# Optimization experiments

Measured on AMD Instinct MI355X. Metric: run time of the kernel, lower is better.

## Reference

```python
import jax, jax.numpy as jnp
import numpy as np

B = 65536; T = 7
N_NUM = 32; N_CAT = 16; CARD = 100; D_CAT = 16
D_STATE = 96; D_HID = 192; S_DIM = 64; DT = 1.0
D_IN = N_NUM + N_CAT * D_CAT + 8  # 296
D_Z = 3 * D_STATE + 64            # 352

def _ln(x, g, b, eps=1e-5):
    m = x.mean(-1, keepdims=True)
    v = ((x - m) ** 2).mean(-1, keepdims=True)
    return (x - m) * jax.lax.rsqrt(v + eps) * g + b

def _gelu(x):
    return jax.nn.gelu(x, approximate=False)  # matches torch F.gelu default (erf)

def _forward(x_num, x_static, cat_emb, day_emb, xproj_w, xproj_b, h0,
             bln_g, bln_b, fc1_w, fc1_b, fc2_w, fc2_b,
             spln_g, spln_b, sp1_w, sp1_b, sp2_w, sp2_b,
             base_w, base_b, hln_g, hln_b,
             hm1_w, hm1_b, hm2_w, hm2_b,
             hq1_w, hq1_b, hq2_w, hq2_b,
             hn1_w, hn1_b, hn2_w, hn2_b, x_cat):
    Bsz = x_num.shape[0]
    # categorical embeddings: per-feature table lookup -> (B,T,N_CAT,D_CAT)
    emb = jax.vmap(lambda tab, idx: tab[idx], in_axes=(0, 2), out_axes=2)(cat_emb, x_cat)
    emb = emb.reshape(Bsz, T, N_CAT * D_CAT)
    # day ids are arange(1,8), shared over batch
    day = jnp.broadcast_to(day_emb[1:8], (Bsz, T, 8))
    x = jnp.concatenate([x_num, emb, day], axis=-1)          # (B,T,D_IN)
    x = x @ xproj_w + xproj_b                                # (B,T,D_STATE)

    def step(h, xt):  # Euler-integrated LN+MLP residual cell (dropout = eval identity)
        z = jnp.concatenate([h, xt], axis=-1)                # (B,2*D_STATE)
        z = _ln(z, bln_g, bln_b)
        dh = _gelu(z @ fc1_w + fc1_b) @ fc2_w + fc2_b
        h = h + DT * dh
        return h, h

    h0b = jnp.broadcast_to(h0, (Bsz, D_STATE))
    _, hs = jax.lax.scan(step, h0b, jnp.swapaxes(x, 0, 1))   # (T,B,D_STATE)
    H = jnp.swapaxes(hs, 0, 1)                               # (B,T,D_STATE)
    h_last = H[:, -1]
    h_mean = H.mean(axis=1)
    h_max = H.max(axis=1)

    s = _ln(x_static, spln_g, spln_b)
    s64 = _gelu(s @ sp1_w + sp1_b) @ sp2_w + sp2_b           # (B,64)

    z = jnp.concatenate([h_last, h_mean, h_max, s64], axis=-1)  # (B,D_Z)
    z = _ln(z, hln_g, hln_b)
    base = x_static @ base_w + base_b                        # (B,)
    mean = base + _gelu(z @ hm1_w + hm1_b) @ hm2_w + hm2_b
    q20 = base + _gelu(z @ hq1_w + hq1_b) @ hq2_w + hq2_b
    neg_logit = _gelu(z @ hn1_w + hn1_b) @ hn2_w + hn2_b
    return mean, q20, neg_logit

def setup_inputs() -> dict:
    key = jax.random.key(0)
    ks = iter(jax.random.split(key, 64))
    def w(shape, scale=0.02):
        return (scale * jax.random.normal(next(ks), shape)).astype(jnp.float32)
    def zz(shape):
        return jnp.zeros(shape, jnp.float32)
    def oo(shape):
        return jnp.ones(shape, jnp.float32)
    inp = {
        "x_num": jax.random.normal(next(ks), (B, T, N_NUM), jnp.float32),
        "x_static": jax.random.normal(next(ks), (B, S_DIM), jnp.float32),
        "x_cat": jax.random.randint(next(ks), (B, T, N_CAT), 0, CARD),
        "cat_emb": w((N_CAT, CARD + 1, D_CAT), 1.0),
        "day_emb": w((8, 8), 1.0),
        "xproj_w": w((D_IN, D_STATE)), "xproj_b": zz((D_STATE,)),
        "h0": zz((D_STATE,)),
        "bln_g": oo((2 * D_STATE,)), "bln_b": zz((2 * D_STATE,)),
        "fc1_w": w((2 * D_STATE, D_HID)), "fc1_b": zz((D_HID,)),
        "fc2_w": w((D_HID, D_STATE)), "fc2_b": zz((D_STATE,)),
        "spln_g": oo((S_DIM,)), "spln_b": zz((S_DIM,)),
        "sp1_w": w((S_DIM, 128)), "sp1_b": zz((128,)),
        "sp2_w": w((128, 64)), "sp2_b": zz((64,)),
        "base_w": w((S_DIM,)), "base_b": zz(()),
        "hln_g": oo((D_Z,)), "hln_b": zz((D_Z,)),
        "hm1_w": w((D_Z, D_HID)), "hm1_b": zz((D_HID,)),
        "hm2_w": w((D_HID,)), "hm2_b": zz(()),
        "hq1_w": w((D_Z, D_HID)), "hq1_b": zz((D_HID,)),
        "hq2_w": w((D_HID,)), "hq2_b": zz(()),
        "hn1_w": w((D_Z, D_HID // 2)), "hn1_b": zz((D_HID // 2,)),
        "hn2_w": w((D_HID // 2,)), "hn2_b": zz(()),
    }
    return inp

def reference(x_num, x_static, x_cat, cat_emb, day_emb, xproj_w, xproj_b, h0,
              bln_g, bln_b, fc1_w, fc1_b, fc2_w, fc2_b,
              spln_g, spln_b, sp1_w, sp1_b, sp2_w, sp2_b,
              base_w, base_b, hln_g, hln_b,
              hm1_w, hm1_b, hm2_w, hm2_b,
              hq1_w, hq1_b, hq2_w, hq2_b,
              hn1_w, hn1_b, hn2_w, hn2_b):
    return _forward(x_num, x_static, cat_emb, day_emb, xproj_w, xproj_b, h0,
                    bln_g, bln_b, fc1_w, fc1_b, fc2_w, fc2_b,
                    spln_g, spln_b, sp1_w, sp1_b, sp2_w, sp2_b,
                    base_w, base_b, hln_g, hln_b,
                    hm1_w, hm1_b, hm2_w, hm2_b,
                    hq1_w, hq1_b, hq2_w, hq2_b,
                    hn1_w, hn1_b, hn2_w, hn2_b, x_cat)
```

## Files before the change

kernel.cpp:

```cpp
#include <hip/hip_runtime.h>
#include <math.h>

#define NB 65536

typedef __attribute__((ext_vector_type(8))) short bf16x8;
typedef __attribute__((ext_vector_type(4))) float f32x4;

#define O_BIAST  0
#define O_FC1C   4096
#define O_FC1BP  8192
#define O_FC1FR  12288
#define O_FC2FR  86016
#define O_HDFR   122880
#define O_HDC    460800
#define O_HDBP   462848
#define O_W2C    464896
#define O_SPC    466944
#define O_SPB    467968
#define O_SP1FR  468992
#define O_SP2FR  485376
#define O_XP2FR  501760
#define O_EMB16  557056
#define O_FEAT   608768
#define O_S64    38357504
#define O_STAT   46746112
#define O_BASE   47270400
#define O_XROW   47532544
#define O_XSTAT  135612928

__device__ __forceinline__ unsigned short f2b(float x) {
  unsigned int u = __float_as_uint(x);
  u += 0x7fffu + ((u >> 16) & 1u);
  return (unsigned short)(u >> 16);
}
__device__ __forceinline__ float b2f(unsigned short u) {
  return __uint_as_float(((unsigned)u) << 16);
}
__device__ __forceinline__ float geluf(float x) {
  float z = x * x;
  float e = __builtin_amdgcn_exp2f(-x * (2.3022137f + 0.10294456f * z));
  return x * __builtin_amdgcn_rcpf(1.0f + e);
}

__device__ __forceinline__ void head_fold_part(
    int part, int tid,
    const float* __restrict__ hln_g, const float* __restrict__ hln_b,
    const float* __restrict__ hm1_w, const float* __restrict__ hm1_b,
    const float* __restrict__ hq1_w, const float* __restrict__ hq1_b,
    const float* __restrict__ hn1_w, const float* __restrict__ hn1_b,
    const float* __restrict__ hm2_w, const float* __restrict__ hq2_w,
    const float* __restrict__ hn2_w, char* __restrict__ wsb)
{
  if (tid >= 480) return;
  const int gcol = part*120 + (tid >> 2);
  const int ksl = tid & 3;
  float C = 0.f, Bp = 0.f;
  for (int j = 0; j < 88; ++j) {
    int k = ksl*88 + j;
    float w;
    if (gcol < 192) w = hm1_w[k*192 + gcol];
    else if (gcol < 384) w = hq1_w[k*192 + (gcol-192)];
    else w = hn1_w[k*96 + (gcol-384)];
    C = fmaf(hln_g[k], w, C);
    Bp = fmaf(hln_b[k], w, Bp);
  }
  C += __shfl_xor(C, 1, 64); C += __shfl_xor(C, 2, 64);
  Bp += __shfl_xor(Bp, 1, 64); Bp += __shfl_xor(Bp, 2, 64);
  if (ksl == 0) {
    float b0, w2;
    if (gcol < 192) { b0 = hm1_b[gcol]; w2 = hm2_w[gcol]; }
    else if (gcol < 384) { b0 = hq1_b[gcol-192]; w2 = hq2_w[gcol-192]; }
    else { b0 = hn1_b[gcol-384]; w2 = hn2_w[gcol-384]; }
    ((float*)(wsb + O_HDC))[gcol] = C;
    ((float*)(wsb + O_HDBP))[gcol] = Bp + b0;
    ((float*)(wsb + O_W2C))[gcol] = w2;
  }
}

__global__ void k0_pre(
    const float* __restrict__ cat_emb, const float* __restrict__ day_emb,
    const float* __restrict__ xproj_w, const float* __restrict__ xproj_b,
    const float* __restrict__ bln_g, const float* __restrict__ bln_b,
    const float* __restrict__ fc1_w, const float* __restrict__ fc1_b,
    const float* __restrict__ fc2_w,
    const float* __restrict__ spln_g, const float* __restrict__ spln_b,
    const float* __restrict__ sp1_w, const float* __restrict__ sp1_b,
    const float* __restrict__ sp2_w,
    const float* __restrict__ hln_g, const float* __restrict__ hln_b,
    const float* __restrict__ hm1_w, const float* __restrict__ hm1_b,
    const float* __restrict__ hq1_w, const float* __restrict__ hq1_b,
    const float* __restrict__ hn1_w, const float* __restrict__ hn1_b,
    const float* __restrict__ hm2_w, const float* __restrict__ hq2_w,
    const float* __restrict__ hn2_w,
    char* __restrict__ wsb)
{
  const int b = blockIdx.x, tid = threadIdx.x;
  if (b < 7) {
    if (tid < 96) {
      int t = b;
      float acc = xproj_b[tid];
      #pragma unroll
      for (int d = 0; d < 8; ++d)
        acc = fmaf(day_emb[(1+t)*8 + d], xproj_w[(288+d)*96 + tid], acc);
      ((float*)(wsb + O_BIAST))[t*96 + tid] = acc;
    }
  } else if (b < 9) {
    if (tid < 384) {
      int col = (b-7)*96 + (tid >> 2);
      int ksl = tid & 3;
      float C = 0.f, Bp = 0.f;
      for (int j = 0; j < 48; ++j) {
        int k = ksl*48 + j;
        float w = fc1_w[k*192 + col];
        C = fmaf(bln_g[k], w, C);
        Bp = fmaf(bln_b[k], w, Bp);
      }
      C += __shfl_xor(C, 1, 64); C += __shfl_xor(C, 2, 64);
      Bp += __shfl_xor(Bp, 1, 64); Bp += __shfl_xor(Bp, 2, 64);
      if (ksl == 0) {
        ((float*)(wsb + O_FC1C))[col] = C;
        ((float*)(wsb + O_FC1BP))[col] = Bp + fc1_b[col];
      }
    }
  } else if (b < 81) {
    int seg = b - 9, nt = seg / 6, ks = seg - nt*6;
    int ln = tid >> 3, j = tid & 7;
    int k = ks*32 + (ln>>4)*8 + j, col = nt*16 + (ln&15);
    ((unsigned short*)(wsb + O_FC1FR))[(seg*64 + ln)*8 + j] = f2b(bln_g[k]*fc1_w[k*192 + col]);
  } else if (b < 117) {
    int seg = b - 81, nt = seg / 6, ks = seg - nt*6;
    int ln = tid >> 3, j = tid & 7;
    int k = ks*32 + (ln>>4)*8 + j, col = nt*16 + (ln&15);
    ((unsigned short*)(wsb + O_FC2FR))[(seg*64 + ln)*8 + j] = f2b(fc2_w[k*96 + col]);
  } else if (b < 447) {
    int seg = b - 117, nt = seg / 11, ks = seg - nt*11;
    int ln = tid >> 3, j = tid & 7;
    int k = ks*32 + (ln>>4)*8 + j, gcol = nt*16 + (ln&15);
    float w;
    if (gcol < 192) w = hm1_w[k*192 + gcol];
    else if (gcol < 384) w = hq1_w[k*192 + (gcol-192)];
    else w = hn1_w[k*96 + (gcol-384)];
    ((unsigned short*)(wsb + O_HDFR))[(seg*64 + ln)*8 + j] = f2b(hln_g[k]*w);
  } else if (b < 448) {
    head_fold_part(0, tid, hln_g, hln_b, hm1_w, hm1_b, hq1_w, hq1_b,
                   hn1_w, hn1_b, hm2_w, hq2_w, hn2_w, wsb);
  } else if (b < 449) {
    if (tid < 128) {
      int col = tid;
      float C = 0.f, Bp = sp1_b[col];
      for (int k = 0; k < 64; ++k) {
        float w = sp1_w[k*128 + col];
        C += b2f(f2b(spln_g[k]*w));
        Bp = fmaf(spln_b[k], w, Bp);
      }
      ((float*)(wsb + O_SPC))[col] = C;
      ((float*)(wsb + O_SPB))[col] = Bp;
    }
  } else if (b < 465) {
    int seg = b - 449;
    int ln = tid >> 3, j = tid & 7;
    int nt = seg >> 1, ks = seg & 1;
    int k = ks*32 + (ln>>4)*8 + j, col = nt*16 + (ln&15);
    ((unsigned short*)(wsb + O_SP1FR))[(seg*64 + ln)*8 + j] = f2b(spln_g[k]*sp1_w[k*128 + col]);
  } else if (b < 481) {
    int seg = b - 465;
    int ln = tid >> 3, j = tid & 7;
    int ks = seg & 3;
    int k = ks*32 + (ln>>4)*8 + j, col = (seg >> 2)*16 + (ln&15);
    ((unsigned short*)(wsb + O_SP2FR))[(seg*64 + ln)*8 + j] = f2b(sp2_w[k*64 + col]);
  } else if (b < 535) {
    int seg = b - 481, ks = seg / 6, nt = seg - ks*6;
    int ln = tid >> 3, j = tid & 7;
    int k = ks*32 + (ln>>4)*8 + j, col = nt*16 + (ln&15);
    ((unsigned short*)(wsb + O_XP2FR))[(seg*64 + ln)*8 + j] = f2b(xproj_w[k*96 + col]);
  } else if (b < 586) {
    int i = (b - 535)*512 + tid;
    if (i < 25856)
      ((unsigned short*)(wsb + O_EMB16))[i] = f2b(cat_emb[i]);
  } else {
    head_fold_part(b - 585, tid, hln_g, hln_b, hm1_w, hm1_b, hq1_w, hq1_b,
                   hn1_w, hn1_b, hm2_w, hq2_w, hn2_w, wsb);
  }
}

__global__ __launch_bounds__(256) void k1ab(
    const float* __restrict__ x_num, const int* __restrict__ x_cat,
    const float* __restrict__ x_static, const float* __restrict__ sp2_b,
    const float* __restrict__ base_w, const float* __restrict__ base_b,
    char* __restrict__ wsb, unsigned short* __restrict__ xrow,
    float* __restrict__ xstat)
{
  __shared__ char smem[28288];
  const int tid = threadIdx.x;
  const int wv = tid >> 6, l = tid & 63, lr = l & 15, lq = l >> 4;
  const f32x4 zero4 = {0.f, 0.f, 0.f, 0.f};

  if (blockIdx.x >= 3584) {
    unsigned short* hid = (unsigned short*)smem;
    const int srow = (blockIdx.x - 3584)*64 + wv*16;

    float x0f[8], x1f[8];
    {
      const float* xr = x_static + (size_t)(srow + lr)*64;
      *(float4*)&x0f[0] = *(const float4*)(xr + lq*8);
      *(float4*)&x0f[4] = *(const float4*)(xr + lq*8 + 4);
      *(float4*)&x1f[0] = *(const float4*)(xr + 32 + lq*8);
      *(float4*)&x1f[4] = *(const float4*)(xr + 32 + lq*8 + 4);
    }
    float sm = 0.f, sq = 0.f, bp = 0.f;
    #pragma unroll
    for (int j = 0; j < 8; ++j) {
      sm += x0f[j] + x1f[j];
      sq = fmaf(x0f[j], x0f[j], fmaf(x1f[j], x1f[j], sq));
      bp = fmaf(x0f[j], base_w[lq*8 + j], fmaf(x1f[j], base_w[32 + lq*8 + j], bp));
    }
    sm += __shfl_xor(sm, 16, 64); sm += __shfl_xor(sm, 32, 64);
    sq += __shfl_xor(sq, 16, 64); sq += __shfl_xor(sq, 32, 64);
    bp += __shfl_xor(bp, 16, 64); bp += __shfl_xor(bp, 32, 64);
    if (lq == 0) ((float*)(wsb + O_BASE))[srow + lr] = bp + base_b[0];
    const float ms = sm*(1.f/64.f);
    const float rs = rsqrtf(sq*(1.f/64.f) - ms*ms + 1e-5f);
    float mr[4], rr[4];
    #pragma unroll
    for (int i = 0; i < 4; ++i) {
      mr[i] = __shfl(ms, lq*4 + i, 16);
      rr[i] = __shfl(rs, lq*4 + i, 16);
    }
    union { bf16x8 v; unsigned short u[8]; } ua0, ua1;
    #pragma unroll
    for (int j = 0; j < 8; ++j) { ua0.u[j] = f2b(x0f[j]); ua1.u[j] = f2b(x1f[j]); }

    const bf16x8* f1 = (const bf16x8*)(wsb + O_SP1FR);
    const bf16x8* f2 = (const bf16x8*)(wsb + O_SP2FR);
    unsigned short* hw = hid + wv*2176;

    f32x4 acc[8];
    #pragma unroll
    for (int nt = 0; nt < 8; ++nt) acc[nt] = zero4;
    #pragma unroll
    for (int nt = 0; nt < 8; ++nt) {
      acc[nt] = __builtin_amdgcn_mfma_f32_16x16x32_bf16(ua0.v, f1[(nt*2 + 0)*64 + l], acc[nt], 0, 0, 0);
      acc[nt] = __builtin_amdgcn_mfma_f32_16x16x32_bf16(ua1.v, f1[(nt*2 + 1)*64 + l], acc[nt], 0, 0, 0);
    }
    {
      const float* spC = (const float*)(wsb + O_SPC);
      const float* spB = (const float*)(wsb + O_SPB);
      #pragma unroll
      for (int nt = 0; nt < 8; ++nt) {
        float Cv = spC[nt*16 + lr], Bv = spB[nt*16 + lr];
        #pragma unroll
        for (int i = 0; i < 4; ++i) {
          float hv = rr[i]*(acc[nt][i] - mr[i]*Cv) + Bv;
          hw[(lq*4 + i)*136 + nt*16 + lr] = f2b(geluf(hv));
        }
      }
    }
    f32x4 a2[4];
    #pragma unroll
    for (int nt = 0; nt < 4; ++nt) a2[nt] = zero4;
    #pragma unroll
    for (int ks = 0; ks < 4; ++ks) {
      bf16x8 a = *(const bf16x8*)(hw + lr*136 + ks*32 + lq*8);
      #pragma unroll
      for (int nt = 0; nt < 4; ++nt)
        a2[nt] = __builtin_amdgcn_mfma_f32_16x16x32_bf16(a, f2[(nt*4 + ks)*64 + l], a2[nt], 0, 0, 0);
    }
    float ss[4] = {0.f,0.f,0.f,0.f}, qq[4] = {0.f,0.f,0.f,0.f};
    {
      unsigned short* s64p = (unsigned short*)(wsb + O_S64);
      #pragma unroll
      for (int nt = 0; nt < 4; ++nt) {
        float bv = sp2_b[nt*16 + lr];
        #pragma unroll
        for (int i = 0; i < 4; ++i) {
          unsigned short rb = f2b(a2[nt][i] + bv);
          s64p[(size_t)(srow + lq*4 + i)*64 + nt*16 + lr] = rb;
          float f = b2f(rb);
          ss[i] += f; qq[i] = fmaf(f, f, qq[i]);
        }
      }
    }
    #pragma unroll
    for (int i = 0; i < 4; ++i) {
      ss[i] += __shfl_xor(ss[i], 1, 64); ss[i] += __shfl_xor(ss[i], 2, 64);
      ss[i] += __shfl_xor(ss[i], 4, 64); ss[i] += __shfl_xor(ss[i], 8, 64);
      qq[i] += __shfl_xor(qq[i], 1, 64); qq[i] += __shfl_xor(qq[i], 2, 64);
      qq[i] += __shfl_xor(qq[i], 4, 64); qq[i] += __shfl_xor(qq[i], 8, 64);
    }
    if (lr == 0) {
      float* stat = (float*)(wsb + O_STAT);
      #pragma unroll
      for (int i = 0; i < 4; ++i) {
        size_t r = (size_t)srow + lq*4 + i;
        float2 o; o.x = ss[i]; o.y = qq[i];
        *(float2*)(stat + r*2) = o;
      }
    }
    return;
  }

  float (*ctile)[16][100] = (float(*)[16][100])smem;
  float (*bsh)[96] = (float(*)[96])(smem + 25600);
  const unsigned ctA = blockIdx.x*128u + wv*32u + lr;
  const unsigned ctB = ctA + 16u;
  const int lqh = lq >> 1, lql = lq & 1;

  if (tid < 168)
    ((float4*)bsh)[tid] = ((const float4*)(wsb + O_BIAST))[tid];
  __syncthreads();

  int eA[8], eB[8];
  {
    const int4* ip = (const int4*)(x_cat + (size_t)ctA*16);
    int4 v0 = ip[0], v1 = ip[1], v2 = ip[2], v3 = ip[3];
    eA[0] = lqh ? v0.y : v0.x;  eA[1] = lqh ? v0.w : v0.z;
    eA[2] = lqh ? v1.y : v1.x;  eA[3] = lqh ? v1.w : v1.z;
    eA[4] = lqh ? v2.y : v2.x;  eA[5] = lqh ? v2.w : v2.z;
    eA[6] = lqh ? v3.y : v3.x;  eA[7] = lqh ? v3.w : v3.z;
  }
  {
    const int4* ip = (const int4*)(x_cat + (size_t)ctB*16);
    int4 v0 = ip[0], v1 = ip[1], v2 = ip[2], v3 = ip[3];
    eB[0] = lqh ? v0.y : v0.x;  eB[1] = lqh ? v0.w : v0.z;
    eB[2] = lqh ? v1.y : v1.x;  eB[3] = lqh ? v1.w : v1.z;
    eB[4] = lqh ? v2.y : v2.x;  eB[5] = lqh ? v2.w : v2.z;
    eB[6] = lqh ? v3.y : v3.x;  eB[7] = lqh ? v3.w : v3.z;
  }
  const unsigned short* emb = (const unsigned short*)(wsb + O_EMB16);
  const bf16x8* xp2 = (const bf16x8*)(wsb + O_XP2FR);
  f32x4 accA[6], accB[6];
  #pragma unroll
  for (int nt = 0; nt < 6; ++nt) { accA[nt] = zero4; accB[nt] = zero4; }

  {
    union { bf16x8 v; unsigned short u[8]; } auA, auB;
    {
      const float* xa = x_num + (size_t)ctA*32 + lq*8;
      const float* xb = x_num + (size_t)ctB*32 + lq*8;
      float fa[8], fb[8];
      *(float4*)&fa[0] = *(const float4*)xa;
      *(float4*)&fa[4] = *(const float4*)(xa + 4);
      *(float4*)&fb[0] = *(const float4*)xb;
      *(float4*)&fb[4] = *(const float4*)(xb + 4);
      #pragma unroll
      for (int j = 0; j < 8; ++j) { auA.u[j] = f2b(fa[j]); auB.u[j] = f2b(fb[j]); }
    }
    #pragma unroll
    for (int nt = 0; nt < 6; ++nt) {
      bf16x8 w = xp2[nt*64 + l];
      accA[nt] = __builtin_amdgcn_mfma_f32_16x16x32_bf16(auA.v, w, accA[nt], 0, 0, 0);
      accB[nt] = __builtin_amdgcn_mfma_f32_16x16x32_bf16(auB.v, w, accB[nt], 0, 0, 0);
    }
  }
  #pragma unroll
  for (int c2 = 0; c2 < 8; ++c2) {
    bf16x8 aA = *(const bf16x8*)(emb + ((c2*2+lqh)*101 + eA[c2])*16 + lql*8);
    bf16x8 aB = *(const bf16x8*)(emb + ((c2*2+lqh)*101 + eB[c2])*16 + lql*8);
    #pragma unroll
    for (int nt = 0; nt < 6; ++nt) {
      bf16x8 w = xp2[((c2+1)*6+nt)*64 + l];
      accA[nt] = __builtin_amdgcn_mfma_f32_16x16x32_bf16(aA, w, accA[nt], 0, 0, 0);
      accB[nt] = __builtin_amdgcn_mfma_f32_16x16x32_bf16(aB, w, accB[nt], 0, 0, 0);
    }
  }

  #pragma unroll
  for (int nt = 0; nt < 6; ++nt) {
    #pragma unroll
    for (int i = 0; i < 4; ++i)
      ctile[wv][lq*4 + i][nt*16 + lr] = accA[nt][i];
  }
  asm volatile("s_waitcnt lgkmcnt(0)" ::: "memory");
  __builtin_amdgcn_sched_barrier(0);
  {
    const unsigned t = ctA % 7u;
    float cv[24], bv[24];
    #pragma unroll
    for (int q = 0; q < 6; ++q) {
      *(float4*)&cv[q*4] = *(const float4*)&ctile[wv][lr][lq*24 + q*4];
      *(float4*)&bv[q*4] = *(const float4*)&bsh[t][lq*24 + q*4];
    }
    unsigned ow[12];
    float sm = 0.f, sq = 0.f;
    #pragma unroll
    for (int u = 0; u < 12; ++u) {
      unsigned short u0 = f2b(cv[2*u]   + bv[2*u]);
      unsigned short u1 = f2b(cv[2*u+1] + bv[2*u+1]);
      ow[u] = (unsigned)u0 | ((unsigned)u1 << 16);
      float f0 = b2f(u0), f1 = b2f(u1);
      sm += f0 + f1; sq = fmaf(f0, f0, fmaf(f1, f1, sq));
    }
    {
      uint4* xo = (uint4*)(xrow + (size_t)ctA*96 + lq*24);
      xo[0] = make_uint4(ow[0], ow[1], ow[2], ow[3]);
      xo[1] = make_uint4(ow[4], ow[5], ow[6], ow[7]);
      xo[2] = make_uint4(ow[8], ow[9], ow[10], ow[11]);
    }
    sm += __shfl_xor(sm, 16, 64); sm += __shfl_xor(sm, 32, 64);
    sq += __shfl_xor(sq, 16, 64); sq += __shfl_xor(sq, 32, 64);
    if (lq == 0) {
      float2 o; o.x = sm; o.y = sq;
      *(float2*)(xstat + (size_t)ctA*2) = o;
    }
  }
  asm volatile("s_waitcnt lgkmcnt(0)" ::: "memory");
  __builtin_amdgcn_sched_barrier(0);
  #pragma unroll
  for (int nt = 0; nt < 6; ++nt) {
    #pragma unroll
    for (int i = 0; i < 4; ++i)
      ctile[wv][lq*4 + i][nt*16 + lr] = accB[nt][i];
  }
  asm volatile("s_waitcnt lgkmcnt(0)" ::: "memory");
  __builtin_amdgcn_sched_barrier(0);
  {
    const unsigned t = ctB % 7u;
    float cv[24], bv[24];
    #pragma unroll
    for (int q = 0; q < 6; ++q) {
      *(float4*)&cv[q*4] = *(const float4*)&ctile[wv][lr][lq*24 + q*4];
      *(float4*)&bv[q*4] = *(const float4*)&bsh[t][lq*24 + q*4];
    }
    unsigned ow[12];
    float sm = 0.f, sq = 0.f;
    #pragma unroll
    for (int u = 0; u < 12; ++u) {
      unsigned short u0 = f2b(cv[2*u]   + bv[2*u]);
      unsigned short u1 = f2b(cv[2*u+1] + bv[2*u+1]);
      ow[u] = (unsigned)u0 | ((unsigned)u1 << 16);
      float f0 = b2f(u0), f1 = b2f(u1);
      sm += f0 + f1; sq = fmaf(f0, f0, fmaf(f1, f1, sq));
    }
    {
      uint4* xo = (uint4*)(xrow + (size_t)ctB*96 + lq*24);
      xo[0] = make_uint4(ow[0], ow[1], ow[2], ow[3]);
      xo[1] = make_uint4(ow[4], ow[5], ow[6], ow[7]);
      xo[2] = make_uint4(ow[8], ow[9], ow[10], ow[11]);
    }
    sm += __shfl_xor(sm, 16, 64); sm += __shfl_xor(sm, 32, 64);
    sq += __shfl_xor(sq, 16, 64); sq += __shfl_xor(sq, 32, 64);
    if (lq == 0) {
      float2 o; o.x = sm; o.y = sq;
      *(float2*)(xstat + (size_t)ctB*2) = o;
    }
  }
}

__global__ __launch_bounds__(512, 2) void k1_scan(
    const float* __restrict__ h0, const float* __restrict__ fc2_b,
    const char* __restrict__ wsb, const unsigned short* __restrict__ xrow,
    const float* __restrict__ xstat, unsigned short* __restrict__ feat,
    float* __restrict__ statg)
{
  extern __shared__ char smem[];
  unsigned short* zg = (unsigned short*)smem;
  unsigned short* f1f = (unsigned short*)(smem + 51200);
  unsigned short* f2f = (unsigned short*)(smem + 124928);

  const int tid = threadIdx.x;
  const int wv = tid >> 6;
  const int l = tid & 63;
  const int lr = l & 15;
  const int lq = l >> 4;
  const int rowt = wv*16 + lr;

  {
    const uint4* s1 = (const uint4*)(wsb + O_FC1FR);
    uint4* d1 = (uint4*)f1f;
    for (int o = tid; o < 4608; o += 512) d1[o] = s1[o];
    const uint4* s2 = (const uint4*)(wsb + O_FC2FR);
    uint4* d2 = (uint4*)f2f;
    for (int o = tid; o < 2304; o += 512) d2[o] = s2[o];
  }
  const bf16x8* f1v = (const bf16x8*)f1f;
  const bf16x8* f2v = (const bf16x8*)f2f;

  float C1[12], B1[12];
  {
    const float* fc1C = (const float*)(wsb + O_FC1C);
    const float* fc1BP = (const float*)(wsb + O_FC1BP);
    #pragma unroll
    for (int nt = 0; nt < 12; ++nt) { C1[nt] = fc1C[nt*16+lr]; B1[nt] = fc1BP[nt*16+lr]; }
  }
  float fb2[6];
  #pragma unroll
  for (int nt = 0; nt < 6; ++nt) fb2[nt] = fc2_b[nt*16+lr];

  float h[24], hs[24], hm[24];
  #pragma unroll
  for (int nt = 0; nt < 6; ++nt) {
    float v = h0[nt*16+lr];
    #pragma unroll
    for (int i = 0; i < 4; ++i) { h[nt*4+i] = v; hs[nt*4+i] = 0.f; hm[nt*4+i] = -3.4e38f; }
  }
  __syncthreads();

  const f32x4 zero4 = {0.f, 0.f, 0.f, 0.f};
  const size_t srow_q = (size_t)blockIdx.x*128 + wv*16;

  for (int t = 0; t < 7; ++t) {
    float hsm[4] = {0.f,0.f,0.f,0.f}, hsq[4] = {0.f,0.f,0.f,0.f};
    #pragma unroll
    for (int nt = 0; nt < 6; ++nt) {
      #pragma unroll
      for (int i = 0; i < 4; ++i) {
        unsigned short hb = f2b(h[nt*4+i]);
        zg[(wv*16 + lq*4 + i)*200 + nt*16 + lr] = hb;
        float hf = b2f(hb);
        hsm[i] += hf; hsq[i] = fmaf(hf, hf, hsq[i]);
      }
    }
    #pragma unroll
    for (int i = 0; i < 4; ++i) {
      hsm[i] += __shfl_xor(hsm[i], 1, 64); hsm[i] += __shfl_xor(hsm[i], 2, 64);
      hsm[i] += __shfl_xor(hsm[i], 4, 64); hsm[i] += __shfl_xor(hsm[i], 8, 64);
      hsq[i] += __shfl_xor(hsq[i], 1, 64); hsq[i] += __shfl_xor(hsq[i], 2, 64);
      hsq[i] += __shfl_xor(hsq[i], 4, 64); hsq[i] += __shfl_xor(hsq[i], 8, 64);
    }
    float mr[4], rr[4];
    #pragma unroll
    for (int i = 0; i < 4; ++i) {
      const float2 xs = *(const float2*)(xstat + ((srow_q + lq*4 + i)*7 + t)*2);
      float m = (hsm[i] + xs.x) * (1.f/192.f);
      float var = (hsq[i] + xs.y) * (1.f/192.f) - m*m;
      mr[i] = m; rr[i] = rsqrtf(var + 1e-5f);
    }
    bf16x8 ax[3];
    {
      const unsigned short* xp = xrow + ((srow_q + lr)*7 + t)*96;
      #pragma unroll
      for (int k3 = 0; k3 < 3; ++k3)
        ax[k3] = *(const bf16x8*)(xp + k3*32 + lq*8);
    }
    f32x4 acc[12];
    #pragma unroll
    for (int nt = 0; nt < 12; ++nt) acc[nt] = zero4;
    #pragma unroll
    for (int ks = 0; ks < 3; ++ks) {
      bf16x8 a = *(const bf16x8*)(zg + rowt*200 + ks*32 + lq*8);
      #pragma unroll
      for (int nt = 0; nt < 12; ++nt)
        acc[nt] = __builtin_amdgcn_mfma_f32_16x16x32_bf16(a, f1v[(nt*6+ks)*64 + l], acc[nt], 0, 0, 0);
    }
    #pragma unroll
    for (int k3 = 0; k3 < 3; ++k3) {
      #pragma unroll
      for (int nt = 0; nt < 12; ++nt)
        acc[nt] = __builtin_amdgcn_mfma_f32_16x16x32_bf16(ax[k3], f1v[(nt*6+k3+3)*64 + l], acc[nt], 0, 0, 0);
    }
    #pragma unroll
    for (int nt = 0; nt < 12; ++nt) {
      #pragma unroll
      for (int i = 0; i < 4; ++i) {
        float hid = rr[i]*(acc[nt][i] - mr[i]*C1[nt]) + B1[nt];
        zg[(wv*16 + lq*4 + i)*200 + nt*16 + lr] = f2b(geluf(hid));
      }
    }
    f32x4 a2[6];
    #pragma unroll
    for (int nt = 0; nt < 6; ++nt) a2[nt] = zero4;
    #pragma unroll
    for (int ks = 0; ks < 6; ++ks) {
      bf16x8 a = *(const bf16x8*)(zg + rowt*200 + ks*32 + lq*8);
      #pragma unroll
      for (int nt = 0; nt < 6; ++nt)
        a2[nt] = __builtin_amdgcn_mfma_f32_16x16x32_bf16(a, f2v[(nt*6+ks)*64 + l], a2[nt], 0, 0, 0);
    }
    #pragma unroll
    for (int nt = 0; nt < 6; ++nt) {
      #pragma unroll
      for (int i = 0; i < 4; ++i) {
        int u = nt*4 + i;
        h[u] += a2[nt][i] + fb2[nt];
        hs[u] += h[u];
        hm[u] = fmaxf(hm[u], h[u]);
      }
    }
  }
  float st[4] = {0.f,0.f,0.f,0.f}, qt[4] = {0.f,0.f,0.f,0.f};
  #pragma unroll
  for (int nt = 0; nt < 6; ++nt) {
    #pragma unroll
    for (int i = 0; i < 4; ++i) {
      size_t r = (srow_q + lq*4 + i)*288;
      int c = nt*16 + lr;
      unsigned short b0 = f2b(h[nt*4+i]);
      unsigned short b1 = f2b(hs[nt*4+i]*(1.f/7.f));
      unsigned short b2v = f2b(hm[nt*4+i]);
      feat[r + c] = b0;
      feat[r + 96 + c] = b1;
      feat[r + 192 + c] = b2v;
      float f0 = b2f(b0), f1 = b2f(b1), f2v = b2f(b2v);
      st[i] += f0 + f1 + f2v;
      qt[i] = fmaf(f0, f0, fmaf(f1, f1, fmaf(f2v, f2v, qt[i])));
    }
  }
  #pragma unroll
  for (int i = 0; i < 4; ++i) {
    st[i] += __shfl_xor(st[i], 1, 64); st[i] += __shfl_xor(st[i], 2, 64);
    st[i] += __shfl_xor(st[i], 4, 64); st[i] += __shfl_xor(st[i], 8, 64);
    qt[i] += __shfl_xor(qt[i], 1, 64); qt[i] += __shfl_xor(qt[i], 2, 64);
    qt[i] += __shfl_xor(qt[i], 4, 64); qt[i] += __shfl_xor(qt[i], 8, 64);
  }
  if (lr == 0) {
    #pragma unroll
    for (int i = 0; i < 4; ++i) {
      size_t r = srow_q + lq*4 + i;
      float2 fs = *(float2*)(statg + r*2);
      float stot = fs.x + st[i], qtot = fs.y + qt[i];
      float m = stot*(1.f/352.f);
      float var = qtot*(1.f/352.f) - m*m;
      float2 o; o.x = m; o.y = rsqrtf(var + 1e-5f);
      *(float2*)(statg + r*2) = o;
    }
  }
}

__global__ __launch_bounds__(512, 2) void k2b_heads(
    const float* __restrict__ hm2_b, const float* __restrict__ hq2_b,
    const float* __restrict__ hn2_b, const char* __restrict__ wsb,
    const unsigned short* __restrict__ feat, float* __restrict__ out)
{
  extern __shared__ char smem[];
  const int g = blockIdx.y;
  const int tid = threadIdx.x;
  const int wv = tid >> 6, l = tid & 63, lr = l & 15, lq = l >> 4;
  const int ntn = (g == 2) ? 6 : 12;
  {
    const uint4* src = (const uint4*)(wsb + O_HDFR + (size_t)g*135168);
    uint4* dst = (uint4*)smem;
    const int n = ntn*11*64;
    for (int o = tid; o < n; o += 512) dst[o] = src[o];
  }
  __syncthreads();
  const bf16x8* wfr = (const bf16x8*)smem;
  const float* hdC = (const float*)(wsb + O_HDC);
  const float* hdB = (const float*)(wsb + O_HDBP);
  const float* w2c = (const float*)(wsb + O_W2C);
  const float* stat = (const float*)(wsb + O_STAT);
  const float* baseb = (const float*)(wsb + O_BASE);
  const unsigned short* s64p = (const unsigned short*)(wsb + O_S64);
  const float hb = (g == 0) ? hm2_b[0] : (g == 1) ? hq2_b[0] : hn2_b[0];
  const f32x4 zero4 = {0.f, 0.f, 0.f, 0.f};

  for (int c = blockIdx.x; c < 256; c += gridDim.x) {
    const int base = c*256 + wv*32;
    bf16x8 afr0[11], afr1[11];
    {
      const unsigned short* fr0 = feat + (size_t)(base + lr)*288;
      const unsigned short* fr1 = feat + (size_t)(base + 16 + lr)*288;
      #pragma unroll
      for (int ks = 0; ks < 9; ++ks) {
        afr0[ks] = *(const bf16x8*)(fr0 + ks*32 + lq*8);
        afr1[ks] = *(const bf16x8*)(fr1 + ks*32 + lq*8);
      }
      const unsigned short* sr0 = s64p + (size_t)(base + lr)*64;
      const unsigned short* sr1 = s64p + (size_t)(base + 16 + lr)*64;
      afr0[9]  = *(const bf16x8*)(sr0 + lq*8);
      afr0[10] = *(const bf16x8*)(sr0 + 32 + lq*8);
      afr1[9]  = *(const bf16x8*)(sr1 + lq*8);
      afr1[10] = *(const bf16x8*)(sr1 + 32 + lq*8);
    }
    float mr0[4], rr0[4], mr1[4], rr1[4];
    #pragma unroll
    for (int i = 0; i < 4; ++i) {
      float2 s0 = *(const float2*)(stat + (size_t)(base + lq*4 + i)*2);
      float2 s1 = *(const float2*)(stat + (size_t)(base + 16 + lq*4 + i)*2);
      mr0[i] = s0.x; rr0[i] = s0.y; mr1[i] = s1.x; rr1[i] = s1.y;
    }
    float pr0[4] = {0.f,0.f,0.f,0.f}, pr1[4] = {0.f,0.f,0.f,0.f};
    for (int nt = 0; nt < ntn; ++nt) {
      const int col = (g*12 + nt)*16 + lr;
      const float Cv = hdC[col], Bv = hdB[col], w2v = w2c[col];
      f32x4 a0 = zero4, a1v = zero4;
      #pragma unroll
      for (int ks = 0; ks < 11; ++ks) {
        bf16x8 b = wfr[(nt*11 + ks)*64 + l];
        a0  = __builtin_amdgcn_mfma_f32_16x16x32_bf16(afr0[ks], b, a0, 0, 0, 0);
        a1v = __builtin_amdgcn_mfma_f32_16x16x32_bf16(afr1[ks], b, a1v, 0, 0, 0);
      }
      #pragma unroll
      for (int i = 0; i < 4; ++i) {
        pr0[i] += geluf(rr0[i]*(a0[i]  - mr0[i]*Cv) + Bv) * w2v;
        pr1[i] += geluf(rr1[i]*(a1v[i] - mr1[i]*Cv) + Bv) * w2v;
      }
    }
    #pragma unroll
    for (int i = 0; i < 4; ++i) {
      float v0 = pr0[i], v1 = pr1[i];
      v0 += __shfl_xor(v0, 1, 64); v0 += __shfl_xor(v0, 2, 64);
      v0 += __shfl_xor(v0, 4, 64); v0 += __shfl_xor(v0, 8, 64);
      v1 += __shfl_xor(v1, 1, 64); v1 += __shfl_xor(v1, 2, 64);
      v1 += __shfl_xor(v1, 4, 64); v1 += __shfl_xor(v1, 8, 64);
      if (lr == 0) {
        int r0 = base + lq*4 + i;
        int r1 = base + 16 + lq*4 + i;
        float b0 = (g < 2) ? baseb[r0] : 0.f;
        float b1 = (g < 2) ? baseb[r1] : 0.f;
        out[(size_t)g*NB + r0] = b0 + hb + v0;
        out[(size_t)g*NB + r1] = b1 + hb + v1;
      }
    }
  }
}

extern "C" void kernel_launch(void* const* d_in, const int* in_sizes, int n_in,
                              void* d_out, int out_size, void* d_ws, size_t ws_size,
                              hipStream_t stream) {
  (void)in_sizes; (void)n_in; (void)out_size; (void)ws_size;
  const float* x_num    = (const float*)d_in[0];
  const float* x_static = (const float*)d_in[1];
  const int*   x_cat    = (const int*)  d_in[2];
  const float* cat_emb  = (const float*)d_in[3];
  const float* day_emb  = (const float*)d_in[4];
  const float* xproj_w  = (const float*)d_in[5];
  const float* xproj_b  = (const float*)d_in[6];
  const float* h0       = (const float*)d_in[7];
  const float* bln_g    = (const float*)d_in[8];
  const float* bln_b    = (const float*)d_in[9];
  const float* fc1_w    = (const float*)d_in[10];
  const float* fc1_b    = (const float*)d_in[11];
  const float* fc2_w    = (const float*)d_in[12];
  const float* fc2_b    = (const float*)d_in[13];
  const float* spln_g   = (const float*)d_in[14];
  const float* spln_b   = (const float*)d_in[15];
  const float* sp1_w    = (const float*)d_in[16];
  const float* sp1_b    = (const float*)d_in[17];
  const float* sp2_w    = (const float*)d_in[18];
  const float* sp2_b    = (const float*)d_in[19];
  const float* base_w   = (const float*)d_in[20];
  const float* base_b   = (const float*)d_in[21];
  const float* hln_g    = (const float*)d_in[22];
  const float* hln_b    = (const float*)d_in[23];
  const float* hm1_w    = (const float*)d_in[24];
  const float* hm1_b    = (const float*)d_in[25];
  const float* hm2_w    = (const float*)d_in[26];
  const float* hm2_b    = (const float*)d_in[27];
  const float* hq1_w    = (const float*)d_in[28];
  const float* hq1_b    = (const float*)d_in[29];
  const float* hq2_w    = (const float*)d_in[30];
  const float* hq2_b    = (const float*)d_in[31];
  const float* hn1_w    = (const float*)d_in[32];
  const float* hn1_b    = (const float*)d_in[33];
  const float* hn2_w    = (const float*)d_in[34];
  const float* hn2_b    = (const float*)d_in[35];

  char* wsb = (char*)d_ws;
  unsigned short* feat = (unsigned short*)(wsb + O_FEAT);
  unsigned short* xrow = (unsigned short*)(wsb + O_XROW);
  float* xstat = (float*)(wsb + O_XSTAT);
  float* statg = (float*)(wsb + O_STAT);
  float* out = (float*)d_out;

  k0_pre<<<589, 512, 0, stream>>>(cat_emb, day_emb, xproj_w, xproj_b,
      bln_g, bln_b, fc1_w, fc1_b, fc2_w, spln_g, spln_b, sp1_w, sp1_b, sp2_w,
      hln_g, hln_b, hm1_w, hm1_b, hq1_w, hq1_b, hn1_w, hn1_b,
      hm2_w, hq2_w, hn2_w, wsb);
  k1ab<<<4608, 256, 0, stream>>>(x_num, x_cat, x_static, sp2_b, base_w, base_b,
      wsb, xrow, xstat);
  k1_scan<<<512, 512, 161792, stream>>>(h0, fc2_b, wsb, xrow, xstat, feat, statg);
  k2b_heads<<<dim3(64, 3), 512, 135168, stream>>>(hm2_b, hq2_b, hn2_b,
      wsb, feat, out);
}
```

Baseline: 278.6 us.

## Fuse prediction heads into scan kernel via shared-memory feature tile

Moves the three head MLPs into the end of the scan kernel. The pooled hidden features and the static embedding are staged per row in shared memory instead of being written to global memory and re-read by a separate heads kernel. Head weight fragments are now read directly from global or L2 rather than staged in LDS, and each wave computes all 30 output column tiles for its 16 rows. This removes a kernel launch and the round trip of the feature buffer through memory. In exchange there is no LDS reuse of the head weights and less row blocking per weight load.

```diff
diff --git a/kernel.cpp b/kernel.cpp
--- a/kernel.cpp
+++ b/kernel.cpp
@@ -448,9 +448,11 @@
 
 __global__ __launch_bounds__(512, 2) void k1_scan(
     const float* __restrict__ h0, const float* __restrict__ fc2_b,
+    const float* __restrict__ hm2_b, const float* __restrict__ hq2_b,
+    const float* __restrict__ hn2_b,
     const char* __restrict__ wsb, const unsigned short* __restrict__ xrow,
-    const float* __restrict__ xstat, unsigned short* __restrict__ feat,
-    float* __restrict__ statg)
+    const float* __restrict__ xstat, float* __restrict__ statg,
+    float* __restrict__ out)
 {
   extern __shared__ char smem[];
   unsigned short* zg = (unsigned short*)smem;
@@ -577,23 +579,33 @@
       }
     }
   }
+
+  __syncthreads();
+  unsigned short* zt = (unsigned short*)smem;
   float st[4] = {0.f,0.f,0.f,0.f}, qt[4] = {0.f,0.f,0.f,0.f};
   #pragma unroll
   for (int nt = 0; nt < 6; ++nt) {
     #pragma unroll
     for (int i = 0; i < 4; ++i) {
-      size_t r = (srow_q + lq*4 + i)*288;
+      int row = wv*16 + lq*4 + i;
       int c = nt*16 + lr;
       unsigned short b0 = f2b(h[nt*4+i]);
       unsigned short b1 = f2b(hs[nt*4+i]*(1.f/7.f));
       unsigned short b2v = f2b(hm[nt*4+i]);
-      feat[r + c] = b0;
-      feat[r + 96 + c] = b1;
-      feat[r + 192 + c] = b2v;
-      float f0 = b2f(b0), f1 = b2f(b1), f2v = b2f(b2v);
-      st[i] += f0 + f1 + f2v;
-      qt[i] = fmaf(f0, f0, fmaf(f1, f1, fmaf(f2v, f2v, qt[i])));
-    }
+      zt[row*360 + c] = b0;
+      zt[row*360 + 96 + c] = b1;
+      zt[row*360 + 192 + c] = b2v;
+      float f0 = b2f(b0), f1 = b2f(b1), f2x = b2f(b2v);
+      st[i] += f0 + f1 + f2x;
+      qt[i] = fmaf(f0, f0, fmaf(f1, f1, fmaf(f2x, f2x, qt[i])));
+    }
+  }
+  {
+    const unsigned short* s64p = (const unsigned short*)(wsb + O_S64);
+    const uint4* sp = (const uint4*)(s64p + (srow_q + lr)*64 + lq*16);
+    uint4 v0 = sp[0], v1 = sp[1];
+    *(uint4*)(zt + (wv*16 + lr)*360 + 288 + lq*16) = v0;
+    *(uint4*)(zt + (wv*16 + lr)*360 + 288 + lq*16 + 8) = v1;
   }
   #pragma unroll
   for (int i = 0; i < 4; ++i) {
@@ -602,104 +614,56 @@
     qt[i] += __shfl_xor(qt[i], 1, 64); qt[i] += __shfl_xor(qt[i], 2, 64);
     qt[i] += __shfl_xor(qt[i], 4, 64); qt[i] += __shfl_xor(qt[i], 8, 64);
   }
-  if (lr == 0) {
-    #pragma unroll
-    for (int i = 0; i < 4; ++i) {
-      size_t r = srow_q + lq*4 + i;
-      float2 fs = *(float2*)(statg + r*2);
-      float stot = fs.x + st[i], qtot = fs.y + qt[i];
-      float m = stot*(1.f/352.f);
-      float var = qtot*(1.f/352.f) - m*m;
-      float2 o; o.x = m; o.y = rsqrtf(var + 1e-5f);
-      *(float2*)(statg + r*2) = o;
-    }
-  }
-}
-
-__global__ __launch_bounds__(512, 2) void k2b_heads(
-    const float* __restrict__ hm2_b, const float* __restrict__ hq2_b,
-    const float* __restrict__ hn2_b, const char* __restrict__ wsb,
-    const unsigned short* __restrict__ feat, float* __restrict__ out)
-{
-  extern __shared__ char smem[];
-  const int g = blockIdx.y;
-  const int tid = threadIdx.x;
-  const int wv = tid >> 6, l = tid & 63, lr = l & 15, lq = l >> 4;
-  const int ntn = (g == 2) ? 6 : 12;
-  {
-    const uint4* src = (const uint4*)(wsb + O_HDFR + (size_t)g*135168);
-    uint4* dst = (uint4*)smem;
-    const int n = ntn*11*64;
-    for (int o = tid; o < n; o += 512) dst[o] = src[o];
-  }
-  __syncthreads();
-  const bf16x8* wfr = (const bf16x8*)smem;
+  float mr[4], rr[4];
+  #pragma unroll
+  for (int i = 0; i < 4; ++i) {
+    const float2 fs = *(const float2*)(statg + (srow_q + lq*4 + i)*2);
+    float stot = fs.x + st[i], qtot = fs.y + qt[i];
+    float m = stot*(1.f/352.f);
+    float var = qtot*(1.f/352.f) - m*m;
+    mr[i] = m; rr[i] = rsqrtf(var + 1e-5f);
+  }
+  const bf16x8* hv = (const bf16x8*)(wsb + O_HDFR);
   const float* hdC = (const float*)(wsb + O_HDC);
   const float* hdB = (const float*)(wsb + O_HDBP);
   const float* w2c = (const float*)(wsb + O_W2C);
-  const float* stat = (const float*)(wsb + O_STAT);
-  const float* baseb = (const float*)(wsb + O_BASE);
-  const unsigned short* s64p = (const unsigned short*)(wsb + O_S64);
-  const float hb = (g == 0) ? hm2_b[0] : (g == 1) ? hq2_b[0] : hn2_b[0];
-  const f32x4 zero4 = {0.f, 0.f, 0.f, 0.f};
-
-  for (int c = blockIdx.x; c < 256; c += gridDim.x) {
-    const int base = c*256 + wv*32;
-    bf16x8 afr0[11], afr1[11];
-    {
-      const unsigned short* fr0 = feat + (size_t)(base + lr)*288;
-      const unsigned short* fr1 = feat + (size_t)(base + 16 + lr)*288;
-      #pragma unroll
-      for (int ks = 0; ks < 9; ++ks) {
-        afr0[ks] = *(const bf16x8*)(fr0 + ks*32 + lq*8);
-        afr1[ks] = *(const bf16x8*)(fr1 + ks*32 + lq*8);
-      }
-      const unsigned short* sr0 = s64p + (size_t)(base + lr)*64;
-      const unsigned short* sr1 = s64p + (size_t)(base + 16 + lr)*64;
-      afr0[9]  = *(const bf16x8*)(sr0 + lq*8);
-      afr0[10] = *(const bf16x8*)(sr0 + 32 + lq*8);
-      afr1[9]  = *(const bf16x8*)(sr1 + lq*8);
-      afr1[10] = *(const bf16x8*)(sr1 + 32 + lq*8);
-    }
-    float mr0[4], rr0[4], mr1[4], rr1[4];
+  float p0[4] = {0.f,0.f,0.f,0.f}, p1[4] = {0.f,0.f,0.f,0.f}, p2[4] = {0.f,0.f,0.f,0.f};
+  #pragma unroll
+  for (int nt = 0; nt < 30; ++nt) {
+    const int col = nt*16 + lr;
+    const float Cv = hdC[col], Bv = hdB[col], w2v = w2c[col];
+    f32x4 a0 = zero4;
+    #pragma unroll
+    for (int ks = 0; ks < 11; ++ks) {
+      bf16x8 b = hv[(nt*11 + ks)*64 + l];
+      bf16x8 a = *(const bf16x8*)(zt + (wv*16 + lr)*360 + ks*32 + lq*8);
+      a0 = __builtin_amdgcn_mfma_f32_16x16x32_bf16(a, b, a0, 0, 0, 0);
+    }
     #pragma unroll
     for (int i = 0; i < 4; ++i) {
-      float2 s0 = *(const float2*)(stat + (size_t)(base + lq*4 + i)*2);
-      float2 s1 = *(const float2*)(stat + (size_t)(base + 16 + lq*4 + i)*2);
-      mr0[i] = s0.x; rr0[i] = s0.y; mr1[i] = s1.x; rr1[i] = s1.y;
-    }
-    float pr0[4] = {0.f,0.f,0.f,0.f}, pr1[4] = {0.f,0.f,0.f,0.f};
-    for (int nt = 0; nt < ntn; ++nt) {
-      const int col = (g*12 + nt)*16 + lr;
-      const float Cv = hdC[col], Bv = hdB[col], w2v = w2c[col];
-      f32x4 a0 = zero4, a1v = zero4;
-      #pragma unroll
-      for (int ks = 0; ks < 11; ++ks) {
-        bf16x8 b = wfr[(nt*11 + ks)*64 + l];
-        a0  = __builtin_amdgcn_mfma_f32_16x16x32_bf16(afr0[ks], b, a0, 0, 0, 0);
-        a1v = __builtin_amdgcn_mfma_f32_16x16x32_bf16(afr1[ks], b, a1v, 0, 0, 0);
-      }
-      #pragma unroll
-      for (int i = 0; i < 4; ++i) {
-        pr0[i] += geluf(rr0[i]*(a0[i]  - mr0[i]*Cv) + Bv) * w2v;
-        pr1[i] += geluf(rr1[i]*(a1v[i] - mr1[i]*Cv) + Bv) * w2v;
-      }
-    }
+      float g = geluf(rr[i]*(a0[i] - mr[i]*Cv) + Bv) * w2v;
+      if (nt < 12) p0[i] += g; else if (nt < 24) p1[i] += g; else p2[i] += g;
+    }
+  }
+  #pragma unroll
+  for (int i = 0; i < 4; ++i) {
+    p0[i] += __shfl_xor(p0[i], 1, 64); p0[i] += __shfl_xor(p0[i], 2, 64);
+    p0[i] += __shfl_xor(p0[i], 4, 64); p0[i] += __shfl_xor(p0[i], 8, 64);
+    p1[i] += __shfl_xor(p1[i], 1, 64); p1[i] += __shfl_xor(p1[i], 2, 64);
+    p1[i] += __shfl_xor(p1[i], 4, 64); p1[i] += __shfl_xor(p1[i], 8, 64);
+    p2[i] += __shfl_xor(p2[i], 1, 64); p2[i] += __shfl_xor(p2[i], 2, 64);
+    p2[i] += __shfl_xor(p2[i], 4, 64); p2[i] += __shfl_xor(p2[i], 8, 64);
+  }
+  if (lr == 0) {
+    const float* baseb = (const float*)(wsb + O_BASE);
+    const float hmb = hm2_b[0], hqb = hq2_b[0], hnb = hn2_b[0];
     #pragma unroll
     for (int i = 0; i < 4; ++i) {
-      float v0 = pr0[i], v1 = pr1[i];
-      v0 += __shfl_xor(v0, 1, 64); v0 += __shfl_xor(v0, 2, 64);
-      v0 += __shfl_xor(v0, 4, 64); v0 += __shfl_xor(v0, 8, 64);
-      v1 += __shfl_xor(v1, 1, 64); v1 += __shfl_xor(v1, 2, 64);
-      v1 += __shfl_xor(v1, 4, 64); v1 += __shfl_xor(v1, 8, 64);
-      if (lr == 0) {
-        int r0 = base + lq*4 + i;
-        int r1 = base + 16 + lq*4 + i;
-        float b0 = (g < 2) ? baseb[r0] : 0.f;
-        float b1 = (g < 2) ? baseb[r1] : 0.f;
-        out[(size_t)g*NB + r0] = b0 + hb + v0;
-        out[(size_t)g*NB + r1] = b1 + hb + v1;
-      }
+      size_t r = srow_q + lq*4 + i;
+      float bs = baseb[r];
+      out[r] = bs + hmb + p0[i];
+      out[NB + r] = bs + hqb + p1[i];
+      out[2*NB + r] = hnb + p2[i];
     }
   }
 }
@@ -746,7 +710,6 @@
   const float* hn2_b    = (const float*)d_in[35];
 
   char* wsb = (char*)d_ws;
-  unsigned short* feat = (unsigned short*)(wsb + O_FEAT);
   unsigned short* xrow = (unsigned short*)(wsb + O_XROW);
   float* xstat = (float*)(wsb + O_XSTAT);
   float* statg = (float*)(wsb + O_STAT);
@@ -758,7 +721,6 @@
       hm2_w, hq2_w, hn2_w, wsb);
   k1ab<<<4608, 256, 0, stream>>>(x_num, x_cat, x_static, sp2_b, base_w, base_b,
       wsb, xrow, xstat);
-  k1_scan<<<512, 512, 161792, stream>>>(h0, fc2_b, wsb, xrow, xstat, feat, statg);
-  k2b_heads<<<dim3(64, 3), 512, 135168, stream>>>(hm2_b, hq2_b, hn2_b,
-      wsb, feat, out);
+  k1_scan<<<512, 512, 161792, stream>>>(h0, fc2_b, hm2_b, hq2_b, hn2_b,
+      wsb, xrow, xstat, statg, out);
 }
```

After: 396.8 us. 1.42x slower.
